# Kernel tuning notes

Hardware: AMD Instinct MI355X
Metric: run time of the kernel (lower is better)

Reference implementation:

```python
import jax, jax.numpy as jnp
import numpy as np

N_WORD, N_TOPIC, N_DOC = 30000, 1000, 15000
D_WORD, D_TOPIC, D_OUT = 300, 300, 128
E = dict(ww=800000, wt=400000, wd=600000, td=300000, tt=150000)
SRC_N = dict(ww=N_WORD, wt=N_WORD, wd=N_WORD, td=N_TOPIC, tt=N_TOPIC)
DST_N = dict(ww=N_WORD, wt=N_TOPIC, wd=N_DOC, td=N_DOC, tt=N_TOPIC)


def setup_inputs() -> dict:
    key = jax.random.key(0)
    ks = iter(jax.random.split(key, 64))
    inp = {}
    inp["feat_word"] = jax.random.normal(next(ks), (N_WORD, D_WORD), jnp.float32)
    inp["feat_topic"] = jax.random.normal(next(ks), (N_TOPIC, D_TOPIC), jnp.float32)
    for et in ["ww", "wt", "wd", "td", "tt"]:
        inp[f"{et}_src"] = jax.random.randint(next(ks), (E[et],), 0, SRC_N[et], jnp.int32)
        inp[f"{et}_dst"] = jax.random.randint(next(ks), (E[et],), 0, DST_N[et], jnp.int32)
        inp[f"{et}_w"] = jax.random.uniform(next(ks), (E[et],), jnp.float32)
        din = D_WORD if et[0] == "w" else D_TOPIC
        inp[f"W_{et}"] = jax.random.normal(next(ks), (din, D_OUT), jnp.float32) / np.float32(np.sqrt(din))
        inp[f"b_{et}"] = jnp.zeros((D_OUT,), jnp.float32)
    return inp


def _mean_agg(Wh, src, dst, w, n_dst):
    # DGL fn.u_mul_e('Wh','weight','m') + fn.mean('m','h'): per-edge message
    # Wh[src] * w, mean-reduced per destination node (0 for isolated nodes).
    m = Wh[src] * w[:, None]                                   # [E, D_OUT]
    s = jax.ops.segment_sum(m, dst, num_segments=n_dst)        # [n_dst, D_OUT]
    c = jax.ops.segment_sum(jnp.ones_like(w), dst, num_segments=n_dst)
    return s / jnp.maximum(c, 1.0)[:, None]


def reference(feat_word, feat_topic,
              ww_src, ww_dst, ww_w, wt_src, wt_dst, wt_w,
              wd_src, wd_dst, wd_w, td_src, td_dst, td_w,
              tt_src, tt_dst, tt_w,
              W_ww, b_ww, W_wt, b_wt, W_wd, b_wd, W_td, b_td, W_tt, b_tt):
    # NOTE: the original forward's causal/noise branch is dead code --
    # `Wh = self.weight[etype](feat_dict[srctype])` overwrites it, so the
    # live math is a plain per-edge-type linear projection of source feats.
    Wh_ww = feat_word @ W_ww + b_ww
    Wh_wt = feat_word @ W_wt + b_wt
    Wh_wd = feat_word @ W_wd + b_wd
    Wh_td = feat_topic @ W_td + b_td
    Wh_tt = feat_topic @ W_tt + b_tt
    # multi_update_all(..., 'sum'): sum the per-etype means per dst node type.
    h_word = _mean_agg(Wh_ww, ww_src, ww_dst, ww_w, N_WORD)
    h_topic = (_mean_agg(Wh_wt, wt_src, wt_dst, wt_w, N_TOPIC)
               + _mean_agg(Wh_tt, tt_src, tt_dst, tt_w, N_TOPIC))
    h_doc = (_mean_agg(Wh_wd, wd_src, wd_dst, wd_w, N_DOC)
             + _mean_agg(Wh_td, td_src, td_dst, td_w, N_DOC))
    return (h_word, h_topic, h_doc)
```

## Files before the change

kernel.cpp:

```cpp
#include <hip/hip_runtime.h>

#define N_WORD 30000
#define N_TOPIC 1000
#define N_DOC 15000
#define DIN 300
#define KP 320
#define DOUT 128

#define E_WW 800000
#define E_WT 400000
#define E_WD 600000
#define E_TD 300000
#define E_TT 150000

#define CC_WW 0
#define CC_WT 30000
#define CC_WD 31000
#define CC_TD 46000
#define CC_TT 61000
#define NBINS 62000

#define CAP_WW 80
#define CAP_WT 544
#define CAP_WD 96
#define CAP_TD 56
#define CAP_TT 240
#define SB_WW 0
#define SB_WT (SB_WW + N_WORD * CAP_WW)
#define SB_WD (SB_WT + N_TOPIC * CAP_WT)
#define SB_TD (SB_WD + N_DOC * CAP_WD)
#define SB_TT (SB_TD + N_DOC * CAP_TD)
#define SLOT_TOTAL (SB_TT + N_TOPIC * CAP_TT)

#define CNT_BLOCKS 360
#define HIST_TOTAL 4168000
#define PREPW_BLOCKS 200

#define PFX_BLOCKS 244

#define GW_BLOCKS 469
#define GT_BLOCKS 16

#define PKP 328

#define GB_TOPIC 250
#define GB_DOC 3750
#define GB_WORD 7500

using half8  = __attribute__((ext_vector_type(8))) _Float16;
using half2v = __attribute__((ext_vector_type(2))) _Float16;
using f32x4  = __attribute__((ext_vector_type(4))) float;

struct SegP {
    const int* src[5];
    const int* dst[5];
    const float* w[5];
};

struct WPtrs {
    const float* W[5];
    const float* b[5];
};

__device__ __forceinline__ void decode_grp(
    int b, int& ti, int& hx, int& dlo, int& bins, int& hb,
    int& ch, int& ne, int& cap, int& sbase)
{
    if (b < 64)       { ti=0; hx=b;     dlo=0;     bins=15000; hb=0;       ch=12500; ne=E_WW; cap=CAP_WW; sbase=SB_WW; }
    else if (b < 128) { ti=0; hx=b-64;  dlo=15000; bins=15000; hb=960000;  ch=12500; ne=E_WW; cap=CAP_WW; sbase=SB_WW; }
    else if (b < 192) { ti=1; hx=b-128; dlo=0;     bins=1000;  hb=1920000; ch=6250;  ne=E_WT; cap=CAP_WT; sbase=SB_WT; }
    else if (b < 288) { ti=2; hx=b-192; dlo=0;     bins=15000; hb=1984000; ch=6250;  ne=E_WD; cap=CAP_WD; sbase=SB_WD; }
    else if (b < 336) { ti=3; hx=b-288; dlo=0;     bins=15000; hb=3424000; ch=6250;  ne=E_TD; cap=CAP_TD; sbase=SB_TD; }
    else              { ti=4; hx=b-336; dlo=0;     bins=1000;  hb=4144000; ch=6250;  ne=E_TT; cap=CAP_TT; sbase=SB_TT; }
}

__device__ __forceinline__ void decode_pfx(
    int b, int& hb, int& bins, int& H, int& cb, int& tile)
{
    if (b < 59)       { hb=0;       bins=15000; H=64; cb=0;     tile=b; }
    else if (b < 118) { hb=960000;  bins=15000; H=64; cb=15000; tile=b-59; }
    else if (b < 122) { hb=1920000; bins=1000;  H=64; cb=30000; tile=b-118; }
    else if (b < 181) { hb=1984000; bins=15000; H=96; cb=31000; tile=b-122; }
    else if (b < 240) { hb=3424000; bins=15000; H=48; cb=46000; tile=b-181; }
    else              { hb=4144000; bins=1000;  H=24; cb=61000; tile=b-240; }
}

__global__ __launch_bounds__(1024) void prep_count(
    SegP S, unsigned short* __restrict__ hist,
    WPtrs WP, _Float16* __restrict__ Wt_word, _Float16* __restrict__ Wt_topic,
    float* __restrict__ bcat_word, float* __restrict__ bcat_topic)
{
    __shared__ int h[15000];
    const int b = blockIdx.x;
    if (b < CNT_BLOCKS) {
        int ti, hx, dlo, bins, hb, ch, ne, cap, sbase;
        decode_grp(b, ti, hx, dlo, bins, hb, ch, ne, cap, sbase);
        (void)cap; (void)sbase;
        for (int i = threadIdx.x; i < bins; i += 1024) h[i] = 0;
        __syncthreads();
        const int* __restrict__ dst = S.dst[ti];
        int lo = hx * ch;
        int hiE = lo + ch; if (hiE > ne) hiE = ne;
        for (int i = lo + (int)threadIdx.x; i < hiE; i += 1024) {
            int ld = dst[i] - dlo;
            if ((unsigned)ld < (unsigned)bins) atomicAdd(&h[ld], 1);
        }
        __syncthreads();
        unsigned short* __restrict__ out = hist + hb + hx * bins;
        for (int i = threadIdx.x; i < bins; i += 1024)
            out[i] = (unsigned short)h[i];
    } else {
        int id = (b - CNT_BLOCKS) * 1024 + (int)threadIdx.x;
        const int total = (384 + 256) * KP;
        if (id >= total) return;
        int ng = id / KP;
        int k = id - ng * KP;
        int mat, n, lng;
        _Float16* Wt;
        float* bc;
        if (ng < 384) { lng = ng; mat = lng >> 7; Wt = Wt_word; bc = bcat_word; }
        else          { lng = ng - 384; mat = 3 + (lng >> 7); Wt = Wt_topic; bc = bcat_topic; }
        n = lng & 127;
        Wt[(size_t)lng * KP + k] =
            (k < DIN) ? (_Float16)WP.W[mat][(size_t)k * DOUT + n] : (_Float16)0.f;
        if (k == 0) bc[lng] = WP.b[mat][n];
    }
}

__global__ __launch_bounds__(256) void prefix_k(
    unsigned short* __restrict__ hist, int* __restrict__ cnt)
{
    int hb, bins, H, cb, tile;
    decode_pfx(blockIdx.x, hb, bins, H, cb, tile);
    int g = tile * 256 + (int)threadIdx.x;
    if (g < bins) {
        unsigned short* __restrict__ p = hist + hb + g;
        int run = 0;
        for (int h0 = 0; h0 < H; h0 += 8) {
            int v[8];
#pragma unroll
            for (int j = 0; j < 8; ++j) v[j] = p[(size_t)(h0 + j) * bins];
#pragma unroll
            for (int j = 0; j < 8; ++j) {
                p[(size_t)(h0 + j) * bins] = (unsigned short)run;
                run += v[j];
            }
        }
        cnt[cb + g] = run;
    }
}

template <int NJW>
__device__ __forceinline__ void gemm_cs(
    const float* __restrict__ A, int M,
    const _Float16* __restrict__ Wt, const float* __restrict__ bcat,
    _Float16* __restrict__ C, int Cstride, int rowBlk,
    _Float16* __restrict__ ldsA)
{
    const int t = threadIdx.x;
    const int lane = t & 63;
    const int w = t >> 6;
    const int lm = lane & 15;
    const int lq = lane >> 4;
    const int rowBase = rowBlk * 64;
    const int wc = w * (NJW * 16);

#pragma unroll
    for (int i = 0; i < 10; ++i) {
        int id = i * 256 + t;
        int row = id / 40;
        int c8 = id - row * 40;
        int k = c8 * 8;
        int grow = rowBase + row;
        half8 hv = half8{0, 0, 0, 0, 0, 0, 0, 0};
        if (grow < M) {
            const float* ap = A + (size_t)grow * DIN + k;
            if (k + 8 <= DIN) {
                float4 f0 = *(const float4*)ap;
                float4 f1 = *(const float4*)(ap + 4);
                hv = half8{(_Float16)f0.x, (_Float16)f0.y, (_Float16)f0.z,
                           (_Float16)f0.w, (_Float16)f1.x, (_Float16)f1.y,
                           (_Float16)f1.z, (_Float16)f1.w};
            } else if (k < DIN) {
#pragma unroll
                for (int j = 0; j < 8; ++j)
                    if (k + j < DIN) hv[j] = (_Float16)ap[j];
            }
        }
        *(half8*)&ldsA[row * PKP + k] = hv;
    }
    __syncthreads();

    f32x4 acc[4][NJW];
#pragma unroll
    for (int rt = 0; rt < 4; ++rt)
#pragma unroll
        for (int j = 0; j < NJW; ++j) acc[rt][j] = f32x4{0.f, 0.f, 0.f, 0.f};

#pragma unroll
    for (int s = 0; s < 10; ++s) {
        const int k0 = s * 32 + lq * 8;
        half8 bf[NJW];
#pragma unroll
        for (int j = 0; j < NJW; ++j)
            bf[j] = *(const half8*)&Wt[(size_t)(wc + j * 16 + lm) * KP + k0];
        half8 af[4];
#pragma unroll
        for (int rt = 0; rt < 4; ++rt)
            af[rt] = *(const half8*)&ldsA[(rt * 16 + lm) * PKP + k0];
#pragma unroll
        for (int rt = 0; rt < 4; ++rt)
#pragma unroll
            for (int j = 0; j < NJW; ++j)
                acc[rt][j] = __builtin_amdgcn_mfma_f32_16x16x32_f16(
                    af[rt], bf[j], acc[rt][j], 0, 0, 0);
    }

#pragma unroll
    for (int j = 0; j < NJW; ++j) {
        int col = wc + j * 16 + lm;
        float bias = bcat[col];
#pragma unroll
        for (int rt = 0; rt < 4; ++rt) {
#pragma unroll
            for (int reg = 0; reg < 4; ++reg) {
                int gr = rowBase + rt * 16 + lq * 4 + reg;
                if (gr < M)
                    C[(size_t)gr * Cstride + col] =
                        (_Float16)(acc[rt][j][reg] + bias);
            }
        }
    }
}

__global__ __launch_bounds__(256, 3) void place_gemm(
    SegP S, const unsigned short* __restrict__ hist,
    unsigned int* __restrict__ slots,
    const float* __restrict__ featw, const _Float16* __restrict__ Wtw,
    const float* __restrict__ bw, _Float16* __restrict__ Cw,
    const float* __restrict__ featt, const _Float16* __restrict__ Wtt,
    const float* __restrict__ bt, _Float16* __restrict__ Ct)
{
    __shared__ __align__(16) int usmem[10496];
    const int b = blockIdx.x;
    if (b < CNT_BLOCKS) {
        int ti, hx, dlo, bins, hb, ch, ne, cap, sbase;
        decode_grp(b, ti, hx, dlo, bins, hb, ch, ne, cap, sbase);
        const unsigned int* __restrict__ po32 =
            (const unsigned int*)(hist + hb + hx * bins);
        int nw = bins >> 1;
        for (int j = threadIdx.x; j < nw; j += 256)
            usmem[j] = (int)po32[j];
        __syncthreads();
        const int* __restrict__ dst = S.dst[ti];
        const int* __restrict__ srcp = S.src[ti];
        const float* __restrict__ wp = S.w[ti];
        int lo = hx * ch;
        int hiE = lo + ch; if (hiE > ne) hiE = ne;
        for (int i0 = lo + (int)threadIdx.x; i0 < hiE; i0 += 1024) {
#pragma unroll
            for (int u = 0; u < 4; ++u) {
                int i = i0 + u * 256;
                if (i < hiE) {
                    int d = dst[i];
                    int ld = d - dlo;
                    if ((unsigned)ld < (unsigned)bins) {
                        int sh = (ld & 1) << 4;
                        int old = atomicAdd(&usmem[ld >> 1], 1 << sh);
                        int pos = (old >> sh) & 0xFFFF;
                        if (pos < cap) {
                            unsigned short hw = __builtin_bit_cast(
                                unsigned short, (_Float16)wp[i]);
                            slots[(size_t)sbase + (size_t)d * cap + pos] =
                                (unsigned int)srcp[i] | ((unsigned int)hw << 16);
                        }
                    }
                }
            }
        }
    } else if (b < CNT_BLOCKS + GW_BLOCKS) {
        gemm_cs<6>(featw, N_WORD, Wtw, bw, Cw, 384, b - CNT_BLOCKS,
                   (_Float16*)usmem);
    } else {
        gemm_cs<4>(featt, N_TOPIC, Wtt, bt, Ct, 256,
                   b - CNT_BLOCKS - GW_BLOCKS, (_Float16*)usmem);
    }
}

#define SV2(v, i) __builtin_shufflevector(v, v, i, i + 1)

__device__ __forceinline__ _Float16 wbits(unsigned int q)
{
    return __builtin_bit_cast(_Float16, (unsigned short)(q >> 16));
}

__device__ __forceinline__ void seg_mean16(
    const unsigned int* __restrict__ slots, int beg, int ce, int c,
    const _Float16* __restrict__ rowbase, int strideh, int ln, int sub,
    float a[8])
{
    half2v ac0 = half2v{0, 0}, ac1 = half2v{0, 0};
    half2v ac2 = half2v{0, 0}, ac3 = half2v{0, 0};
    int e = 0;
    for (; e + 16 <= ce; e += 16) {
        unsigned int q0 = slots[beg + e + 0 + sub];
        unsigned int q1 = slots[beg + e + 4 + sub];
        unsigned int q2 = slots[beg + e + 8 + sub];
        unsigned int q3 = slots[beg + e + 12 + sub];
        half8 v0 = *(const half8*)(rowbase + (size_t)(q0 & 0xFFFFu) * strideh + ln * 8);
        half8 v1 = *(const half8*)(rowbase + (size_t)(q1 & 0xFFFFu) * strideh + ln * 8);
        half8 v2 = *(const half8*)(rowbase + (size_t)(q2 & 0xFFFFu) * strideh + ln * 8);
        half8 v3 = *(const half8*)(rowbase + (size_t)(q3 & 0xFFFFu) * strideh + ln * 8);
        _Float16 h0 = wbits(q0), h1 = wbits(q1), h2 = wbits(q2), h3 = wbits(q3);
        half2v w0 = half2v{h0, h0}, w1 = half2v{h1, h1};
        half2v w2 = half2v{h2, h2}, w3 = half2v{h3, h3};
        ac0 += SV2(v0, 0) * w0 + SV2(v1, 0) * w1 + SV2(v2, 0) * w2 + SV2(v3, 0) * w3;
        ac1 += SV2(v0, 2) * w0 + SV2(v1, 2) * w1 + SV2(v2, 2) * w2 + SV2(v3, 2) * w3;
        ac2 += SV2(v0, 4) * w0 + SV2(v1, 4) * w1 + SV2(v2, 4) * w2 + SV2(v3, 4) * w3;
        ac3 += SV2(v0, 6) * w0 + SV2(v1, 6) * w1 + SV2(v2, 6) * w2 + SV2(v3, 6) * w3;
    }
    for (int e2 = e + sub; e2 < ce; e2 += 4) {
        unsigned int q = slots[beg + e2];
        half8 v = *(const half8*)(rowbase + (size_t)(q & 0xFFFFu) * strideh + ln * 8);
        _Float16 h = wbits(q);
        half2v wp = half2v{h, h};
        ac0 += SV2(v, 0) * wp;
        ac1 += SV2(v, 2) * wp;
        ac2 += SV2(v, 4) * wp;
        ac3 += SV2(v, 6) * wp;
    }
    a[0] = (float)ac0.x; a[1] = (float)ac0.y;
    a[2] = (float)ac1.x; a[3] = (float)ac1.y;
    a[4] = (float)ac2.x; a[5] = (float)ac2.y;
    a[6] = (float)ac3.x; a[7] = (float)ac3.y;
#pragma unroll
    for (int j = 0; j < 8; ++j) {
        a[j] += __shfl_down(a[j], 16);
        a[j] += __shfl_down(a[j], 32);
    }
    float inv = 1.0f / (float)(c > 1 ? c : 1);
#pragma unroll
    for (int j = 0; j < 8; ++j) a[j] *= inv;
}

__global__ __launch_bounds__(256) void gather_all(
    const unsigned int* __restrict__ slots, const int* __restrict__ cnt,
    const _Float16* __restrict__ Wh_word, const _Float16* __restrict__ Wh_topic,
    float* __restrict__ out_word, float* __restrict__ out_topic,
    float* __restrict__ out_doc)
{
    const int b = blockIdx.x;
    const int t = threadIdx.x;
    const int lane = t & 63;
    const int wv = t >> 6;
    const int sub = lane >> 4;
    const int ln = lane & 15;

    float a[8];
    float* outp;
    int node;

    if (b < GB_TOPIC) {
        node = b * 4 + wv;
        int c1 = cnt[CC_WT + node];
        int ce1 = c1 < CAP_WT ? c1 : CAP_WT;
        seg_mean16(slots, SB_WT + node * CAP_WT, ce1, c1, Wh_word + 128, 384, ln, sub, a);
        int c2 = cnt[CC_TT + node];
        int ce2 = c2 < CAP_TT ? c2 : CAP_TT;
        float a2[8];
        seg_mean16(slots, SB_TT + node * CAP_TT, ce2, c2, Wh_topic + 128, 256, ln, sub, a2);
#pragma unroll
        for (int j = 0; j < 8; ++j) a[j] += a2[j];
        outp = out_topic;
    } else if (b < GB_TOPIC + GB_DOC) {
        node = (b - GB_TOPIC) * 4 + wv;
        int c1 = cnt[CC_WD + node];
        int ce1 = c1 < CAP_WD ? c1 : CAP_WD;
        seg_mean16(slots, SB_WD + node * CAP_WD, ce1, c1, Wh_word + 256, 384, ln, sub, a);
        int c2 = cnt[CC_TD + node];
        int ce2 = c2 < CAP_TD ? c2 : CAP_TD;
        float a2[8];
        seg_mean16(slots, SB_TD + node * CAP_TD, ce2, c2, Wh_topic, 256, ln, sub, a2);
#pragma unroll
        for (int j = 0; j < 8; ++j) a[j] += a2[j];
        outp = out_doc;
    } else {
        node = (b - GB_TOPIC - GB_DOC) * 4 + wv;
        int c = cnt[CC_WW + node];
        int ce = c < CAP_WW ? c : CAP_WW;
        seg_mean16(slots, SB_WW + node * CAP_WW, ce, c, Wh_word, 384, ln, sub, a);
        outp = out_word;
    }

    if (sub == 0) {
        float4* o = (float4*)outp + (size_t)node * 32 + ln * 2;
        o[0] = make_float4(a[0], a[1], a[2], a[3]);
        o[1] = make_float4(a[4], a[5], a[6], a[7]);
    }
}

extern "C" void kernel_launch(void* const* d_in, const int* in_sizes, int n_in,
                              void* d_out, int out_size, void* d_ws, size_t ws_size,
                              hipStream_t stream)
{
    const float* feat_word  = (const float*)d_in[0];
    const float* feat_topic = (const float*)d_in[1];

    const int*   ww_src = (const int*)d_in[2];
    const int*   ww_dst = (const int*)d_in[3];
    const float* ww_w   = (const float*)d_in[4];
    const float* W_ww   = (const float*)d_in[5];
    const float* b_ww   = (const float*)d_in[6];

    const int*   wt_src = (const int*)d_in[7];
    const int*   wt_dst = (const int*)d_in[8];
    const float* wt_w   = (const float*)d_in[9];
    const float* W_wt   = (const float*)d_in[10];
    const float* b_wt   = (const float*)d_in[11];

    const int*   wd_src = (const int*)d_in[12];
    const int*   wd_dst = (const int*)d_in[13];
    const float* wd_w   = (const float*)d_in[14];
    const float* W_wd   = (const float*)d_in[15];
    const float* b_wd   = (const float*)d_in[16];

    const int*   td_src = (const int*)d_in[17];
    const int*   td_dst = (const int*)d_in[18];
    const float* td_w   = (const float*)d_in[19];
    const float* W_td   = (const float*)d_in[20];
    const float* b_td   = (const float*)d_in[21];

    const int*   tt_src = (const int*)d_in[22];
    const int*   tt_dst = (const int*)d_in[23];
    const float* tt_w   = (const float*)d_in[24];
    const float* W_tt   = (const float*)d_in[25];
    const float* b_tt   = (const float*)d_in[26];

    char* wsb = (char*)d_ws;
    size_t off = 0;
    _Float16* Wh_word  = (_Float16*)(wsb + off); off += (size_t)N_WORD * 384 * 2;
    _Float16* Wh_topic = (_Float16*)(wsb + off); off += (size_t)N_TOPIC * 256 * 2;
    _Float16* Wt_word  = (_Float16*)(wsb + off); off += (size_t)384 * KP * 2;
    _Float16* Wt_topic = (_Float16*)(wsb + off); off += (size_t)256 * KP * 2;
    float* bcat_word   = (float*)(wsb + off);    off += 384 * 4;
    float* bcat_topic  = (float*)(wsb + off);    off += 256 * 4;
    unsigned int* slots = (unsigned int*)(wsb + off); off += (size_t)SLOT_TOTAL * 4;
    int* cnt_all       = (int*)(wsb + off);      off += (size_t)NBINS * 4;
    unsigned short* hist = (unsigned short*)(wsb + off); off += (size_t)HIST_TOTAL * 2;

    float* out_word  = (float*)d_out;
    float* out_topic = out_word + (size_t)N_WORD * DOUT;
    float* out_doc   = out_topic + (size_t)N_TOPIC * DOUT;

    SegP S;
    S.src[0] = ww_src; S.dst[0] = ww_dst; S.w[0] = ww_w;
    S.src[1] = wt_src; S.dst[1] = wt_dst; S.w[1] = wt_w;
    S.src[2] = wd_src; S.dst[2] = wd_dst; S.w[2] = wd_w;
    S.src[3] = td_src; S.dst[3] = td_dst; S.w[3] = td_w;
    S.src[4] = tt_src; S.dst[4] = tt_dst; S.w[4] = tt_w;

    WPtrs WP;
    WP.W[0] = W_ww; WP.W[1] = W_wt; WP.W[2] = W_wd; WP.W[3] = W_td; WP.W[4] = W_tt;
    WP.b[0] = b_ww; WP.b[1] = b_wt; WP.b[2] = b_wd; WP.b[3] = b_td; WP.b[4] = b_tt;

    prep_count<<<CNT_BLOCKS + PREPW_BLOCKS, 1024, 0, stream>>>(
        S, hist, WP, Wt_word, Wt_topic, bcat_word, bcat_topic);
    prefix_k<<<PFX_BLOCKS, 256, 0, stream>>>(hist, cnt_all);
    place_gemm<<<CNT_BLOCKS + GW_BLOCKS + GT_BLOCKS, 256, 0, stream>>>(
        S, hist, slots,
        feat_word, Wt_word, bcat_word, Wh_word,
        feat_topic, Wt_topic, bcat_topic, Wh_topic);
    gather_all<<<GB_TOPIC + GB_DOC + GB_WORD, 256, 0, stream>>>(
        slots, cnt_all, Wh_word, Wh_topic, out_word, out_topic, out_doc);

    (void)in_sizes; (void)n_in; (void)ws_size;
}
```

Measured before the change: 305.2 us.

## Replace fine-grained per-block histograms with two-pass coarse bucket sort

Replaces the per-chunk full-resolution destination histograms (millions of u16 entries) and their column prefix kernel with a coarse bucket count (destination shifted into up to 64 buckets), a single-block prefix scan fused into the GEMM launch, and a two-pass radix-style placement. Pass A scatters packed edges into bucket order in a global staging buffer; pass B does per-node LDS counting within each bucket and writes the slot arrays and counts. This removes the large histogram write/read traffic but adds an extra 18 MB edge staging round trip, one more launch, a serial single-block scan, and edge placement no longer overlaps the GEMM.

```diff
diff --git a/kernel.cpp b/kernel.cpp
--- a/kernel.cpp
+++ b/kernel.cpp
@@ -12,6 +12,7 @@
 #define E_WD 600000
 #define E_TD 300000
 #define E_TT 150000
+#define E_TOTAL 2250000
 
 #define CC_WW 0
 #define CC_WT 30000
@@ -32,15 +33,24 @@
 #define SB_TT (SB_TD + N_DOC * CAP_TD)
 #define SLOT_TOTAL (SB_TT + N_TOPIC * CAP_TT)
 
-#define CNT_BLOCKS 360
-#define HIST_TOTAL 4168000
+#define NB_WW 59
+#define NB_WT 32
+#define NB_WD 30
+#define NB_TD 30
+#define NB_TT 32
+#define CB_WW 0
+#define CB_WT (CB_WW + 64 * NB_WW)
+#define CB_WD (CB_WT + 64 * NB_WT)
+#define CB_TD (CB_WD + 96 * NB_WD)
+#define CB_TT (CB_TD + 48 * NB_TD)
+#define COARSE_TOTAL (CB_TT + 24 * NB_TT)
+#define NBK_TOTAL 183
+
+#define CHUNK_BLOCKS 296
 #define PREPW_BLOCKS 200
-
-#define PFX_BLOCKS 244
 
 #define GW_BLOCKS 469
 #define GT_BLOCKS 16
-
 #define PKP 328
 
 #define GB_TOPIC 250
@@ -62,55 +72,49 @@
     const float* b[5];
 };
 
-__device__ __forceinline__ void decode_grp(
-    int b, int& ti, int& hx, int& dlo, int& bins, int& hb,
-    int& ch, int& ne, int& cap, int& sbase)
-{
-    if (b < 64)       { ti=0; hx=b;     dlo=0;     bins=15000; hb=0;       ch=12500; ne=E_WW; cap=CAP_WW; sbase=SB_WW; }
-    else if (b < 128) { ti=0; hx=b-64;  dlo=15000; bins=15000; hb=960000;  ch=12500; ne=E_WW; cap=CAP_WW; sbase=SB_WW; }
-    else if (b < 192) { ti=1; hx=b-128; dlo=0;     bins=1000;  hb=1920000; ch=6250;  ne=E_WT; cap=CAP_WT; sbase=SB_WT; }
-    else if (b < 288) { ti=2; hx=b-192; dlo=0;     bins=15000; hb=1984000; ch=6250;  ne=E_WD; cap=CAP_WD; sbase=SB_WD; }
-    else if (b < 336) { ti=3; hx=b-288; dlo=0;     bins=15000; hb=3424000; ch=6250;  ne=E_TD; cap=CAP_TD; sbase=SB_TD; }
-    else              { ti=4; hx=b-336; dlo=0;     bins=1000;  hb=4144000; ch=6250;  ne=E_TT; cap=CAP_TT; sbase=SB_TT; }
-}
-
-__device__ __forceinline__ void decode_pfx(
-    int b, int& hb, int& bins, int& H, int& cb, int& tile)
-{
-    if (b < 59)       { hb=0;       bins=15000; H=64; cb=0;     tile=b; }
-    else if (b < 118) { hb=960000;  bins=15000; H=64; cb=15000; tile=b-59; }
-    else if (b < 122) { hb=1920000; bins=1000;  H=64; cb=30000; tile=b-118; }
-    else if (b < 181) { hb=1984000; bins=15000; H=96; cb=31000; tile=b-122; }
-    else if (b < 240) { hb=3424000; bins=15000; H=48; cb=46000; tile=b-181; }
-    else              { hb=4144000; bins=1000;  H=24; cb=61000; tile=b-240; }
-}
-
-__global__ __launch_bounds__(1024) void prep_count(
-    SegP S, unsigned short* __restrict__ hist,
+__device__ __forceinline__ void decode_chunk(
+    int blk, int& ti, int& hx, int& ch, int& ne, int& nb, int& sh, int& cb)
+{
+    if (blk < 64)       { ti=0; hx=blk;     ch=12500; ne=E_WW; nb=NB_WW; sh=9; cb=CB_WW; }
+    else if (blk < 128) { ti=1; hx=blk-64;  ch=6250;  ne=E_WT; nb=NB_WT; sh=5; cb=CB_WT; }
+    else if (blk < 224) { ti=2; hx=blk-128; ch=6250;  ne=E_WD; nb=NB_WD; sh=9; cb=CB_WD; }
+    else if (blk < 272) { ti=3; hx=blk-224; ch=6250;  ne=E_TD; nb=NB_TD; sh=9; cb=CB_TD; }
+    else                { ti=4; hx=blk-272; ch=6250;  ne=E_TT; nb=NB_TT; sh=5; cb=CB_TT; }
+}
+
+__device__ __forceinline__ void decode_bucket(
+    int g, int& b, int& nb, int& nblk, int& sh, int& N,
+    int& cap, int& sb, int& cc, int& cb, int& bee)
+{
+    if (g < 59)       { b=g;     nb=NB_WW; nblk=64; sh=9; N=N_WORD;  cap=CAP_WW; sb=SB_WW; cc=CC_WW; cb=CB_WW; bee=800000; }
+    else if (g < 91)  { b=g-59;  nb=NB_WT; nblk=64; sh=5; N=N_TOPIC; cap=CAP_WT; sb=SB_WT; cc=CC_WT; cb=CB_WT; bee=1200000; }
+    else if (g < 121) { b=g-91;  nb=NB_WD; nblk=96; sh=9; N=N_DOC;   cap=CAP_WD; sb=SB_WD; cc=CC_WD; cb=CB_WD; bee=1800000; }
+    else if (g < 151) { b=g-121; nb=NB_TD; nblk=48; sh=9; N=N_DOC;   cap=CAP_TD; sb=SB_TD; cc=CC_TD; cb=CB_TD; bee=2100000; }
+    else              { b=g-151; nb=NB_TT; nblk=24; sh=5; N=N_TOPIC; cap=CAP_TT; sb=SB_TT; cc=CC_TT; cb=CB_TT; bee=2250000; }
+}
+
+__global__ __launch_bounds__(1024) void count_w(
+    SegP S, int* __restrict__ coarse,
     WPtrs WP, _Float16* __restrict__ Wt_word, _Float16* __restrict__ Wt_topic,
     float* __restrict__ bcat_word, float* __restrict__ bcat_topic)
 {
-    __shared__ int h[15000];
-    const int b = blockIdx.x;
-    if (b < CNT_BLOCKS) {
-        int ti, hx, dlo, bins, hb, ch, ne, cap, sbase;
-        decode_grp(b, ti, hx, dlo, bins, hb, ch, ne, cap, sbase);
-        (void)cap; (void)sbase;
-        for (int i = threadIdx.x; i < bins; i += 1024) h[i] = 0;
+    __shared__ int hh[64];
+    const int blk = blockIdx.x;
+    if (blk < CHUNK_BLOCKS) {
+        int ti, hx, ch, ne, nb, sh, cb;
+        decode_chunk(blk, ti, hx, ch, ne, nb, sh, cb);
+        if (threadIdx.x < 64) hh[threadIdx.x] = 0;
         __syncthreads();
         const int* __restrict__ dst = S.dst[ti];
         int lo = hx * ch;
-        int hiE = lo + ch; if (hiE > ne) hiE = ne;
-        for (int i = lo + (int)threadIdx.x; i < hiE; i += 1024) {
-            int ld = dst[i] - dlo;
-            if ((unsigned)ld < (unsigned)bins) atomicAdd(&h[ld], 1);
-        }
+        int hi = lo + ch; if (hi > ne) hi = ne;
+        for (int i = lo + (int)threadIdx.x; i < hi; i += 1024)
+            atomicAdd(&hh[dst[i] >> sh], 1);
         __syncthreads();
-        unsigned short* __restrict__ out = hist + hb + hx * bins;
-        for (int i = threadIdx.x; i < bins; i += 1024)
-            out[i] = (unsigned short)h[i];
+        if ((int)threadIdx.x < nb)
+            coarse[cb + hx * nb + threadIdx.x] = hh[threadIdx.x];
     } else {
-        int id = (b - CNT_BLOCKS) * 1024 + (int)threadIdx.x;
+        int id = (blk - CHUNK_BLOCKS) * 1024 + (int)threadIdx.x;
         const int total = (384 + 256) * KP;
         if (id >= total) return;
         int ng = id / KP;
@@ -124,29 +128,6 @@
         Wt[(size_t)lng * KP + k] =
             (k < DIN) ? (_Float16)WP.W[mat][(size_t)k * DOUT + n] : (_Float16)0.f;
         if (k == 0) bc[lng] = WP.b[mat][n];
-    }
-}
-
-__global__ __launch_bounds__(256) void prefix_k(
-    unsigned short* __restrict__ hist, int* __restrict__ cnt)
-{
-    int hb, bins, H, cb, tile;
-    decode_pfx(blockIdx.x, hb, bins, H, cb, tile);
-    int g = tile * 256 + (int)threadIdx.x;
-    if (g < bins) {
-        unsigned short* __restrict__ p = hist + hb + g;
-        int run = 0;
-        for (int h0 = 0; h0 < H; h0 += 8) {
-            int v[8];
-#pragma unroll
-            for (int j = 0; j < 8; ++j) v[j] = p[(size_t)(h0 + j) * bins];
-#pragma unroll
-            for (int j = 0; j < 8; ++j) {
-                p[(size_t)(h0 + j) * bins] = (unsigned short)run;
-                run += v[j];
-            }
-        }
-        cnt[cb + g] = run;
     }
 }
 
@@ -233,57 +214,95 @@
     }
 }
 
-__global__ __launch_bounds__(256, 3) void place_gemm(
-    SegP S, const unsigned short* __restrict__ hist,
-    unsigned int* __restrict__ slots,
+__global__ __launch_bounds__(256, 3) void pfx_gemm(
+    int* __restrict__ coarse,
     const float* __restrict__ featw, const _Float16* __restrict__ Wtw,
     const float* __restrict__ bw, _Float16* __restrict__ Cw,
     const float* __restrict__ featt, const _Float16* __restrict__ Wtt,
     const float* __restrict__ bt, _Float16* __restrict__ Ct)
 {
     __shared__ __align__(16) int usmem[10496];
-    const int b = blockIdx.x;
-    if (b < CNT_BLOCKS) {
-        int ti, hx, dlo, bins, hb, ch, ne, cap, sbase;
-        decode_grp(b, ti, hx, dlo, bins, hb, ch, ne, cap, sbase);
-        const unsigned int* __restrict__ po32 =
-            (const unsigned int*)(hist + hb + hx * bins);
-        int nw = bins >> 1;
-        for (int j = threadIdx.x; j < nw; j += 256)
-            usmem[j] = (int)po32[j];
+    const int blk = blockIdx.x;
+    if (blk == 0) {
+        int* ttot = usmem;
+        int* tpfx = usmem + 256;
+        int g = threadIdx.x;
+        int b, nb, nblk, sh, N, cap, sb, cc, cb, bee;
+        if (g < NBK_TOTAL) {
+            decode_bucket(g, b, nb, nblk, sh, N, cap, sb, cc, cb, bee);
+            int tot = 0;
+            for (int k = 0; k < nblk; ++k) tot += coarse[cb + k * nb + b];
+            ttot[g] = tot;
+        }
         __syncthreads();
-        const int* __restrict__ dst = S.dst[ti];
-        const int* __restrict__ srcp = S.src[ti];
-        const float* __restrict__ wp = S.w[ti];
-        int lo = hx * ch;
-        int hiE = lo + ch; if (hiE > ne) hiE = ne;
-        for (int i0 = lo + (int)threadIdx.x; i0 < hiE; i0 += 1024) {
-#pragma unroll
-            for (int u = 0; u < 4; ++u) {
-                int i = i0 + u * 256;
-                if (i < hiE) {
-                    int d = dst[i];
-                    int ld = d - dlo;
-                    if ((unsigned)ld < (unsigned)bins) {
-                        int sh = (ld & 1) << 4;
-                        int old = atomicAdd(&usmem[ld >> 1], 1 << sh);
-                        int pos = (old >> sh) & 0xFFFF;
-                        if (pos < cap) {
-                            unsigned short hw = __builtin_bit_cast(
-                                unsigned short, (_Float16)wp[i]);
-                            slots[(size_t)sbase + (size_t)d * cap + pos] =
-                                (unsigned int)srcp[i] | ((unsigned int)hw << 16);
-                        }
-                    }
-                }
+        if (threadIdx.x == 0) {
+            int run = 0;
+            for (int i = 0; i < NBK_TOTAL; ++i) { tpfx[i] = run; run += ttot[i]; }
+        }
+        __syncthreads();
+        if (g < NBK_TOTAL) {
+            int run = tpfx[g];
+            for (int k = 0; k < nblk; ++k) {
+                int idx = cb + k * nb + b;
+                int v = coarse[idx];
+                coarse[idx] = run;
+                run += v;
             }
         }
-    } else if (b < CNT_BLOCKS + GW_BLOCKS) {
-        gemm_cs<6>(featw, N_WORD, Wtw, bw, Cw, 384, b - CNT_BLOCKS,
+    } else if (blk < 1 + GW_BLOCKS) {
+        gemm_cs<6>(featw, N_WORD, Wtw, bw, Cw, 384, blk - 1,
                    (_Float16*)usmem);
     } else {
-        gemm_cs<4>(featt, N_TOPIC, Wtt, bt, Ct, 256,
-                   b - CNT_BLOCKS - GW_BLOCKS, (_Float16*)usmem);
+        gemm_cs<4>(featt, N_TOPIC, Wtt, bt, Ct, 256, blk - 1 - GW_BLOCKS,
+                   (_Float16*)usmem);
+    }
+}
+
+__global__ __launch_bounds__(1024) void pass_a(
+    SegP S, const int* __restrict__ coarse, int2* __restrict__ BE)
+{
+    __shared__ int cur[64];
+    int ti, hx, ch, ne, nb, sh, cb;
+    decode_chunk(blockIdx.x, ti, hx, ch, ne, nb, sh, cb);
+    if ((int)threadIdx.x < nb)
+        cur[threadIdx.x] = coarse[cb + hx * nb + threadIdx.x];
+    __syncthreads();
+    const int* __restrict__ dst = S.dst[ti];
+    const int* __restrict__ src = S.src[ti];
+    const float* __restrict__ wp = S.w[ti];
+    int lo = hx * ch;
+    int hi = lo + ch; if (hi > ne) hi = ne;
+    for (int i = lo + (int)threadIdx.x; i < hi; i += 1024) {
+        int d = dst[i];
+        int p = atomicAdd(&cur[d >> sh], 1);
+        unsigned short hw = __builtin_bit_cast(unsigned short, (_Float16)wp[i]);
+        BE[p] = make_int2(d, src[i] | ((int)hw << 16));
+    }
+}
+
+__global__ __launch_bounds__(1024) void pass_b(
+    const int* __restrict__ coarse, const int2* __restrict__ BE,
+    unsigned int* __restrict__ slots, int* __restrict__ cnt)
+{
+    __shared__ int cl[512];
+    int b, nb, nblk, sh, N, cap, sb, cc, cb, bee;
+    decode_bucket(blockIdx.x, b, nb, nblk, sh, N, cap, sb, cc, cb, bee);
+    const int width = 1 << sh;
+    const int n0 = b << sh;
+    for (int j = threadIdx.x; j < width; j += 1024) cl[j] = 0;
+    __syncthreads();
+    int st = coarse[cb + b];
+    int en = (b + 1 < nb) ? coarse[cb + b + 1] : bee;
+    for (int i = st + (int)threadIdx.x; i < en; i += 1024) {
+        int2 q = BE[i];
+        int pos = atomicAdd(&cl[q.x - n0], 1);
+        if (pos < cap)
+            slots[(size_t)sb + (size_t)q.x * cap + pos] = (unsigned int)q.y;
+    }
+    __syncthreads();
+    for (int j = threadIdx.x; j < width; j += 1024) {
+        int d = n0 + j;
+        if (d < N) cnt[cc + d] = cl[j];
     }
 }
 
@@ -446,7 +465,8 @@
     float* bcat_topic  = (float*)(wsb + off);    off += 256 * 4;
     unsigned int* slots = (unsigned int*)(wsb + off); off += (size_t)SLOT_TOTAL * 4;
     int* cnt_all       = (int*)(wsb + off);      off += (size_t)NBINS * 4;
-    unsigned short* hist = (unsigned short*)(wsb + off); off += (size_t)HIST_TOTAL * 2;
+    int* coarse        = (int*)(wsb + off);      off += (size_t)COARSE_TOTAL * 4;
+    int2* BE           = (int2*)(wsb + off);     off += (size_t)E_TOTAL * 8;
 
     float* out_word  = (float*)d_out;
     float* out_topic = out_word + (size_t)N_WORD * DOUT;
@@ -463,13 +483,14 @@
     WP.W[0] = W_ww; WP.W[1] = W_wt; WP.W[2] = W_wd; WP.W[3] = W_td; WP.W[4] = W_tt;
     WP.b[0] = b_ww; WP.b[1] = b_wt; WP.b[2] = b_wd; WP.b[3] = b_td; WP.b[4] = b_tt;
 
-    prep_count<<<CNT_BLOCKS + PREPW_BLOCKS, 1024, 0, stream>>>(
-        S, hist, WP, Wt_word, Wt_topic, bcat_word, bcat_topic);
-    prefix_k<<<PFX_BLOCKS, 256, 0, stream>>>(hist, cnt_all);
-    place_gemm<<<CNT_BLOCKS + GW_BLOCKS + GT_BLOCKS, 256, 0, stream>>>(
-        S, hist, slots,
+    count_w<<<CHUNK_BLOCKS + PREPW_BLOCKS, 1024, 0, stream>>>(
+        S, coarse, WP, Wt_word, Wt_topic, bcat_word, bcat_topic);
+    pfx_gemm<<<1 + GW_BLOCKS + GT_BLOCKS, 256, 0, stream>>>(
+        coarse,
         feat_word, Wt_word, bcat_word, Wh_word,
         feat_topic, Wt_topic, bcat_topic, Wh_topic);
+    pass_a<<<CHUNK_BLOCKS, 1024, 0, stream>>>(S, coarse, BE);
+    pass_b<<<NBK_TOTAL, 1024, 0, stream>>>(coarse, BE, slots, cnt_all);
     gather_all<<<GB_TOPIC + GB_DOC + GB_WORD, 256, 0, stream>>>(
         slots, cnt_all, Wh_word, Wh_topic, out_word, out_topic, out_doc);
 
```

After: 301.0 us. About the same (-1.4%).
